# Kernel tuning notes

Measured on AMD Instinct MI355X. Metric: run time of the kernel, lower is better.

Reference implementation:

```python
import jax, jax.numpy as jnp
import numpy as np

HIDDEN = 1024
HEADS = 16
HEAD = HIDDEN // HEADS  # 64, rotary_emb_dim == head dim
B = 8
S = 1024  # max_seqlen; all sequences full length
WINDOW = (64, 64)  # sliding_window=128 -> (64, 64)
ROPE_BASE = 10000.0


def _rope_cos_sin(seqlen, dim, base):
    inv_freq = 1.0 / (base ** (jnp.arange(0, dim, 2, dtype=jnp.float32) / dim))
    t = jnp.arange(seqlen, dtype=jnp.float32)
    freqs = jnp.outer(t, inv_freq)  # [S, dim/2]
    return jnp.cos(freqs), jnp.sin(freqs)


def _apply_rope(x, cos, sin):
    # x: [B, S, H, D], non-interleaved rotary over full head dim
    d2 = cos.shape[-1]
    x1, x2 = x[..., :d2], x[..., d2:]
    c = cos[None, :, None, :]
    s = sin[None, :, None, :]
    return jnp.concatenate([x1 * c - x2 * s, x2 * c + x1 * s], axis=-1)


def setup_inputs() -> dict:
    key = jax.random.key(0)
    k1, k2, k3 = jax.random.split(key, 3)
    hidden_states = jax.random.normal(k1, (B * S, HIDDEN), dtype=jnp.float32)
    cu_seqlens = jnp.arange(B + 1, dtype=jnp.int32) * S
    indices = jnp.arange(B * S, dtype=jnp.int32)
    attn_mask = jnp.ones((B, S), dtype=jnp.int32)
    Wqkv = jax.random.normal(k2, (3 * HIDDEN, HIDDEN), dtype=jnp.float32) * 0.02
    Wo = jax.random.normal(k3, (HIDDEN, HIDDEN), dtype=jnp.float32) * 0.02
    return {
        'hidden_states': hidden_states,
        'cu_seqlens': cu_seqlens,
        'max_seqlen': S,
        'indices': indices,
        'attn_mask': attn_mask,
        'Wqkv': Wqkv,
        'Wo': Wo,
    }


def reference(hidden_states, cu_seqlens, max_seqlen, indices, attn_mask, Wqkv, Wo):
    # QKV projection on unpadded tokens: [T, 3*H*D]
    qkv = hidden_states @ Wqkv.T
    qkv = qkv.reshape(B, S, 3, HEADS, HEAD)
    # Rotary positions reset per sequence; all sequences are full length S.
    cos, sin = _rope_cos_sin(S, HEAD, ROPE_BASE)
    q = _apply_rope(qkv[:, :, 0], cos, sin)
    k = _apply_rope(qkv[:, :, 1], cos, sin)
    v = qkv[:, :, 2]
    scores = jnp.einsum('bshd,bthd->bhst', q, k) / jnp.sqrt(jnp.float32(HEAD))
    # sliding-window mask: key j visible to query i iff i-left <= j <= i+right
    i = jnp.arange(S)[:, None]
    j = jnp.arange(S)[None, :]
    win = (j >= i - WINDOW[0]) & (j <= i + WINDOW[1])  # [S, S]
    key_mask = attn_mask.astype(bool)[:, None, None, :]  # [B,1,1,S]
    mask = win[None, None, :, :] & key_mask
    scores = jnp.where(mask, scores, jnp.finfo(scores.dtype).min)
    probs = jax.nn.softmax(scores, axis=-1)
    attn = jnp.einsum('bhst,bthd->bshd', probs, v).reshape(B * S, HIDDEN)
    return attn @ Wo.T
```

## Files before the change

### kernel.cpp

```cpp
#include <hip/hip_runtime.h>


typedef __attribute__((ext_vector_type(8))) short short8;
typedef __attribute__((ext_vector_type(4))) float f32x4;

#define SEQ   1024
#define NHEAD 16
#define HEADD 64
#define NTOK  8192

__device__ __forceinline__ unsigned short f2bf(float x) {
  unsigned u = __float_as_uint(x);
  u += 0x7fffu + ((u >> 16) & 1u);
  return (unsigned short)(u >> 16);
}

__device__ __forceinline__ void gload_lds16(const void* g, void* l) {
  __builtin_amdgcn_global_load_lds((__attribute__((address_space(1))) void*)(g),
                                   (__attribute__((address_space(3))) void*)(l),
                                   16, 0, 0);
}

__global__ __launch_bounds__(256) void cvt_bf16(const float* __restrict__ in,
                                                unsigned short* __restrict__ out,
                                                int n4) {
  int i = blockIdx.x * 256 + threadIdx.x;
  if (i < n4) {
    float4 v = ((const float4*)in)[i];
    ushort4 o;
    o.x = f2bf(v.x); o.y = f2bf(v.y); o.z = f2bf(v.z); o.w = f2bf(v.w);
    ((ushort4*)out)[i] = o;
  }
}

__global__ __launch_bounds__(256) void gemm_qkv_rope(
    const unsigned short* __restrict__ A,
    const unsigned short* __restrict__ W,
    unsigned short* __restrict__ qb,
    unsigned short* __restrict__ kb,
    unsigned short* __restrict__ vt)
{
  __shared__ unsigned short As[128 * 32];
  __shared__ unsigned short Bs[128 * 32];
  const int tid  = threadIdx.x;
  const int wave = tid >> 6, lane = tid & 63;
  const int quad = lane >> 4, l15 = lane & 15;
  const int row0 = blockIdx.y * 128;
  const int col0 = blockIdx.x * 128;
  const int mrow = (wave >> 1) * 64;
  const int ncol = (wave & 1) * 64;

  f32x4 acc[4][4];
#pragma unroll
  for (int i = 0; i < 4; i++)
#pragma unroll
    for (int j = 0; j < 4; j++) acc[i][j] = (f32x4){0.f, 0.f, 0.f, 0.f};

  for (int k0 = 0; k0 < 1024; k0 += 32) {
#pragma unroll
    for (int i = 0; i < 2; i++) {
      int p = i * 256 + tid;
      int r = p >> 2, c = p & 3;
      gload_lds16(A + (size_t)(row0 + r) * 1024 + k0 + c * 8, &As[p * 8]);
      gload_lds16(W + (size_t)(col0 + r) * 1024 + k0 + c * 8, &Bs[p * 8]);
    }
    __syncthreads();
    short8 af[4], bf[4];
#pragma unroll
    for (int mt = 0; mt < 4; mt++)
      af[mt] = *(const short8*)&As[(mrow + mt * 16 + l15) * 32 + quad * 8];
#pragma unroll
    for (int nt = 0; nt < 4; nt++)
      bf[nt] = *(const short8*)&Bs[(ncol + nt * 16 + l15) * 32 + quad * 8];
#pragma unroll
    for (int mt = 0; mt < 4; mt++)
#pragma unroll
      for (int nt = 0; nt < 4; nt++)
        acc[mt][nt] = __builtin_amdgcn_mfma_f32_16x16x32_bf16(af[mt], bf[nt],
                                                              acc[mt][nt], 0, 0, 0);
    __syncthreads();
  }

  const int colw  = col0 + ncol;
  const int which = colw >> 10;
  const int h     = (colw >> 6) & 15;
  const int rowg  = row0 + mrow;

  if (which == 2) {
#pragma unroll
    for (int mt = 0; mt < 4; mt++) {
      int rbase = rowg + mt * 16 + quad * 4;
      int b = rbase >> 10, s = rbase & 1023;
#pragma unroll
      for (int c = 0; c < 4; c++) {
        int d = c * 16 + l15;
        ushort4 o;
        o.x = f2bf(acc[mt][c][0]); o.y = f2bf(acc[mt][c][1]);
        o.z = f2bf(acc[mt][c][2]); o.w = f2bf(acc[mt][c][3]);
        *(ushort4*)&vt[((size_t)((b * 16 + h) * 64 + d)) * 1024 + s] = o;
      }
    }
  } else {
    unsigned short* dst = (which == 0) ? qb : kb;
    const float scale = (which == 0) ? 0.125f : 1.0f;
    const float kf = 0.41524101186092034f;
    float inv0 = exp2f(-(float)l15 * kf);
    float inv1 = exp2f(-(float)(l15 + 16) * kf);
#pragma unroll
    for (int mt = 0; mt < 4; mt++) {
#pragma unroll
      for (int r = 0; r < 4; r++) {
        int row = rowg + mt * 16 + quad * 4 + r;
        int b = row >> 10, s = row & 1023;
        size_t base = (size_t)((b * 16 + h) * 1024 + s) * 64;
        float sn0, cs0, sn1, cs1;
        sincosf((float)s * inv0, &sn0, &cs0);
        sincosf((float)s * inv1, &sn1, &cs1);
        float x1a = acc[mt][0][r], x2a = acc[mt][2][r];
        float x1b = acc[mt][1][r], x2b = acc[mt][3][r];
        dst[base + l15]           = f2bf((x1a * cs0 - x2a * sn0) * scale);
        dst[base + 32 + l15]      = f2bf((x2a * cs0 + x1a * sn0) * scale);
        dst[base + 16 + l15]      = f2bf((x1b * cs1 - x2b * sn1) * scale);
        dst[base + 48 + l15]      = f2bf((x2b * cs1 + x1b * sn1) * scale);
      }
    }
  }
}

__global__ __launch_bounds__(256) void attn_win(
    const unsigned short* __restrict__ qb,
    const unsigned short* __restrict__ kb,
    const unsigned short* __restrict__ vt,
    const int* __restrict__ am,
    unsigned short* __restrict__ ob)
{
  __shared__ unsigned short Ks[192 * 72];
  __shared__ unsigned short Vs[64 * 200];
  __shared__ unsigned short Ps[4][16 * 200];
  __shared__ unsigned short smask[192];

  const int tid  = threadIdx.x;
  const int wave = tid >> 6, lane = tid & 63;
  const int quad = lane >> 4, l15 = lane & 15;
  const int qs = blockIdx.x * 64;
  const int h  = blockIdx.y, b = blockIdx.z;
  const size_t hb = (size_t)(b * 16 + h);
  const unsigned short* Qg = qb + hb * SEQ * 64;
  const unsigned short* Kg = kb + hb * SEQ * 64;
  const unsigned short* Vg = vt + hb * 64 * SEQ;
  const int t0 = qs - 64;

#pragma unroll
  for (int i = 0; i < 6; i++) {
    int p = i * 256 + tid;
    int r = p >> 3, c = p & 7;
    int t = t0 + r; t = t < 0 ? 0 : (t > 1023 ? 1023 : t);
    *(short8*)&Ks[r * 72 + c * 8] = *(const short8*)&Kg[(size_t)t * 64 + c * 8];
  }
#pragma unroll
  for (int i = 0; i < 6; i++) {
    int p = i * 256 + tid;
    int d = p / 24, c = p % 24;
    int t = t0 + c * 8; t = t < 0 ? 0 : (t > 1016 ? 1016 : t);
    *(short8*)&Vs[d * 200 + c * 8] = *(const short8*)&Vg[(size_t)d * SEQ + t];
  }
  if (tid < 192) {
    int t = t0 + tid;
    smask[tid] = (t >= 0 && t < SEQ) ? (unsigned short)(am[b * SEQ + t] != 0) : 0;
  }
  __syncthreads();

  const int qw = qs + wave * 16;
  short8 qf0 = *(const short8*)&Qg[(size_t)(qw + l15) * 64 + quad * 8];
  short8 qf1 = *(const short8*)&Qg[(size_t)(qw + l15) * 64 + 32 + quad * 8];

  f32x4 sc[12];
#pragma unroll
  for (int tt = 0; tt < 12; tt++) {
    short8 b0 = *(const short8*)&Ks[(tt * 16 + l15) * 72 + quad * 8];
    short8 b1 = *(const short8*)&Ks[(tt * 16 + l15) * 72 + 32 + quad * 8];
    f32x4 a = (f32x4){0.f, 0.f, 0.f, 0.f};
    a = __builtin_amdgcn_mfma_f32_16x16x32_bf16(qf0, b0, a, 0, 0, 0);
    a = __builtin_amdgcn_mfma_f32_16x16x32_bf16(qf1, b1, a, 0, 0, 0);
    sc[tt] = a;
  }

  float lrow[4];
#pragma unroll
  for (int r = 0; r < 4; r++) {
    int i = qw + quad * 4 + r;
    float mx = -3e38f;
#pragma unroll
    for (int tt = 0; tt < 12; tt++) {
      int t = t0 + tt * 16 + l15;
      bool ok = (t >= i - 64) && (t <= i + 64) && smask[tt * 16 + l15];
      float v = ok ? sc[tt][r] : -3e38f;
      sc[tt][r] = v;
      mx = fmaxf(mx, v);
    }
#pragma unroll
    for (int off = 1; off < 16; off <<= 1) mx = fmaxf(mx, __shfl_xor(mx, off));
    float sum = 0.f;
#pragma unroll
    for (int tt = 0; tt < 12; tt++) {
      float p = __expf(sc[tt][r] - mx);
      sc[tt][r] = p;
      sum += p;
    }
#pragma unroll
    for (int off = 1; off < 16; off <<= 1) sum += __shfl_xor(sum, off);
    lrow[r] = sum;
  }

  unsigned short* Pw = Ps[wave];
#pragma unroll
  for (int tt = 0; tt < 12; tt++)
#pragma unroll
    for (int r = 0; r < 4; r++)
      Pw[(quad * 4 + r) * 200 + tt * 16 + l15] = f2bf(sc[tt][r]);
  __syncthreads();

  f32x4 o[4];
#pragma unroll
  for (int dt = 0; dt < 4; dt++) o[dt] = (f32x4){0.f, 0.f, 0.f, 0.f};
#pragma unroll
  for (int kt = 0; kt < 6; kt++) {
    short8 pf = *(const short8*)&Pw[l15 * 200 + kt * 32 + quad * 8];
#pragma unroll
    for (int dt = 0; dt < 4; dt++) {
      short8 vf = *(const short8*)&Vs[(dt * 16 + l15) * 200 + kt * 32 + quad * 8];
      o[dt] = __builtin_amdgcn_mfma_f32_16x16x32_bf16(pf, vf, o[dt], 0, 0, 0);
    }
  }

#pragma unroll
  for (int r = 0; r < 4; r++) {
    float inv = 1.f / lrow[r];
    int tok = b * SEQ + qw + quad * 4 + r;
    size_t base = (size_t)tok * 1024 + h * 64;
#pragma unroll
    for (int dt = 0; dt < 4; dt++)
      ob[base + dt * 16 + l15] = f2bf(o[dt][r] * inv);
  }
}

__global__ __launch_bounds__(256) void gemm_out(
    const unsigned short* __restrict__ A,
    const unsigned short* __restrict__ W,
    float* __restrict__ out)
{
  __shared__ unsigned short As[128 * 32];
  __shared__ unsigned short Bs[128 * 32];
  const int tid  = threadIdx.x;
  const int wave = tid >> 6, lane = tid & 63;
  const int quad = lane >> 4, l15 = lane & 15;
  const int row0 = blockIdx.y * 128;
  const int col0 = blockIdx.x * 128;
  const int mrow = (wave >> 1) * 64;
  const int ncol = (wave & 1) * 64;

  f32x4 acc[4][4];
#pragma unroll
  for (int i = 0; i < 4; i++)
#pragma unroll
    for (int j = 0; j < 4; j++) acc[i][j] = (f32x4){0.f, 0.f, 0.f, 0.f};

  for (int k0 = 0; k0 < 1024; k0 += 32) {
#pragma unroll
    for (int i = 0; i < 2; i++) {
      int p = i * 256 + tid;
      int r = p >> 2, c = p & 3;
      gload_lds16(A + (size_t)(row0 + r) * 1024 + k0 + c * 8, &As[p * 8]);
      gload_lds16(W + (size_t)(col0 + r) * 1024 + k0 + c * 8, &Bs[p * 8]);
    }
    __syncthreads();
    short8 af[4], bf[4];
#pragma unroll
    for (int mt = 0; mt < 4; mt++)
      af[mt] = *(const short8*)&As[(mrow + mt * 16 + l15) * 32 + quad * 8];
#pragma unroll
    for (int nt = 0; nt < 4; nt++)
      bf[nt] = *(const short8*)&Bs[(ncol + nt * 16 + l15) * 32 + quad * 8];
#pragma unroll
    for (int mt = 0; mt < 4; mt++)
#pragma unroll
      for (int nt = 0; nt < 4; nt++)
        acc[mt][nt] = __builtin_amdgcn_mfma_f32_16x16x32_bf16(af[mt], bf[nt],
                                                              acc[mt][nt], 0, 0, 0);
    __syncthreads();
  }

  const int colw = col0 + ncol;
  const int rowg = row0 + mrow;
#pragma unroll
  for (int mt = 0; mt < 4; mt++)
#pragma unroll
    for (int r = 0; r < 4; r++) {
      int row = rowg + mt * 16 + quad * 4 + r;
#pragma unroll
      for (int nt = 0; nt < 4; nt++)
        out[(size_t)row * 1024 + colw + nt * 16 + l15] = acc[mt][nt][r];
    }
}

extern "C" void kernel_launch(void* const* d_in, const int* in_sizes, int n_in,
                              void* d_out, int out_size, void* d_ws, size_t ws_size,
                              hipStream_t stream) {
  const float* hidden = (const float*)d_in[0];
  const int*   am     = (const int*)d_in[4];
  const float* Wqkv   = (const float*)d_in[5];
  const float* Wo     = (const float*)d_in[6];
  float* out = (float*)d_out;

  char* ws = (char*)d_ws;
  unsigned short* hb  = (unsigned short*)(ws);
  unsigned short* wqb = (unsigned short*)(ws + (size_t)(16 << 20));
  unsigned short* wob = (unsigned short*)(ws + (size_t)(22 << 20));
  unsigned short* qbf = (unsigned short*)(ws + (size_t)(24 << 20));
  unsigned short* kbf = (unsigned short*)(ws + (size_t)(40 << 20));
  unsigned short* vtb = (unsigned short*)(ws + (size_t)(56 << 20));
  unsigned short* ab  = hb;

  cvt_bf16<<<(2097152 + 255) / 256, 256, 0, stream>>>(hidden, hb, 2097152);
  cvt_bf16<<<(786432 + 255) / 256, 256, 0, stream>>>(Wqkv, wqb, 786432);
  cvt_bf16<<<(262144 + 255) / 256, 256, 0, stream>>>(Wo, wob, 262144);

  dim3 g1(24, 64);
  gemm_qkv_rope<<<g1, 256, 0, stream>>>(hb, wqb, qbf, kbf, vtb);

  dim3 g2(16, 16, 8);
  attn_win<<<g2, 256, 0, stream>>>(qbf, kbf, vtb, am, ab);

  dim3 g3(8, 64);
  gemm_out<<<g3, 256, 0, stream>>>(ab, wob, out);
}
```

Measured before the change: 254.6 us.

## Merge bf16 conversion kernels and precompute RoPE cos/sin table

Combines the three float-to-bf16 conversion launches into one prep kernel. The same kernel also fills a per-position cos/sin table that the QKV GEMM epilogue reads instead of calling sincosf per element. This is meant to cut launch overhead and the expensive transcendental work in the RoPE epilogue. In exchange the epilogue does extra global loads of the 256KB table, which should mostly hit in cache.

```diff
diff --git a/kernel.cpp b/kernel.cpp
--- a/kernel.cpp
+++ b/kernel.cpp
@@ -21,21 +21,35 @@
                                    16, 0, 0);
 }
 
-__global__ __launch_bounds__(256) void cvt_bf16(const float* __restrict__ in,
-                                                unsigned short* __restrict__ out,
-                                                int n4) {
-  int i = blockIdx.x * 256 + threadIdx.x;
-  if (i < n4) {
-    float4 v = ((const float4*)in)[i];
-    ushort4 o;
-    o.x = f2bf(v.x); o.y = f2bf(v.y); o.z = f2bf(v.z); o.w = f2bf(v.w);
-    ((ushort4*)out)[i] = o;
-  }
+__global__ __launch_bounds__(256) void prep(
+    const float* __restrict__ hidden, const float* __restrict__ Wqkv,
+    const float* __restrict__ Wo,
+    unsigned short* __restrict__ hb, unsigned short* __restrict__ wqb,
+    unsigned short* __restrict__ wob, float2* __restrict__ tab) {
+  int bid = blockIdx.x;
+  const float* in; unsigned short* out; int i;
+  if (bid < 8192)       { in = hidden; out = hb;  i = bid * 256 + threadIdx.x; }
+  else if (bid < 11264) { in = Wqkv;   out = wqb; i = (bid - 8192) * 256 + threadIdx.x; }
+  else if (bid < 12288) { in = Wo;     out = wob; i = (bid - 11264) * 256 + threadIdx.x; }
+  else {
+    int j = (bid - 12288) * 256 + threadIdx.x;
+    int s = j >> 5, d = j & 31;
+    float inv = exp2f(-(float)d * 0.41524101186092034f);
+    float sn, cs;
+    sincosf((float)s * inv, &sn, &cs);
+    tab[j] = make_float2(cs, sn);
+    return;
+  }
+  float4 v = ((const float4*)in)[i];
+  ushort4 o;
+  o.x = f2bf(v.x); o.y = f2bf(v.y); o.z = f2bf(v.z); o.w = f2bf(v.w);
+  ((ushort4*)out)[i] = o;
 }
 
 __global__ __launch_bounds__(256) void gemm_qkv_rope(
     const unsigned short* __restrict__ A,
     const unsigned short* __restrict__ W,
+    const float2* __restrict__ tab,
     unsigned short* __restrict__ qb,
     unsigned short* __restrict__ kb,
     unsigned short* __restrict__ vt)
@@ -103,9 +117,6 @@
   } else {
     unsigned short* dst = (which == 0) ? qb : kb;
     const float scale = (which == 0) ? 0.125f : 1.0f;
-    const float kf = 0.41524101186092034f;
-    float inv0 = exp2f(-(float)l15 * kf);
-    float inv1 = exp2f(-(float)(l15 + 16) * kf);
 #pragma unroll
     for (int mt = 0; mt < 4; mt++) {
 #pragma unroll
@@ -113,15 +124,14 @@
         int row = rowg + mt * 16 + quad * 4 + r;
         int b = row >> 10, s = row & 1023;
         size_t base = (size_t)((b * 16 + h) * 1024 + s) * 64;
-        float sn0, cs0, sn1, cs1;
-        sincosf((float)s * inv0, &sn0, &cs0);
-        sincosf((float)s * inv1, &sn1, &cs1);
+        float2 t0 = tab[s * 32 + l15];
+        float2 t1 = tab[s * 32 + 16 + l15];
         float x1a = acc[mt][0][r], x2a = acc[mt][2][r];
         float x1b = acc[mt][1][r], x2b = acc[mt][3][r];
-        dst[base + l15]           = f2bf((x1a * cs0 - x2a * sn0) * scale);
-        dst[base + 32 + l15]      = f2bf((x2a * cs0 + x1a * sn0) * scale);
-        dst[base + 16 + l15]      = f2bf((x1b * cs1 - x2b * sn1) * scale);
-        dst[base + 48 + l15]      = f2bf((x2b * cs1 + x1b * sn1) * scale);
+        dst[base + l15]           = f2bf((x1a * t0.x - x2a * t0.y) * scale);
+        dst[base + 32 + l15]      = f2bf((x2a * t0.x + x1a * t0.y) * scale);
+        dst[base + 16 + l15]      = f2bf((x1b * t1.x - x2b * t1.y) * scale);
+        dst[base + 48 + l15]      = f2bf((x2b * t1.x + x1b * t1.y) * scale);
       }
     }
   }
@@ -319,14 +329,13 @@
   unsigned short* qbf = (unsigned short*)(ws + (size_t)(24 << 20));
   unsigned short* kbf = (unsigned short*)(ws + (size_t)(40 << 20));
   unsigned short* vtb = (unsigned short*)(ws + (size_t)(56 << 20));
+  float2*         tab = (float2*)(ws + (size_t)(72 << 20));
   unsigned short* ab  = hb;
 
-  cvt_bf16<<<(2097152 + 255) / 256, 256, 0, stream>>>(hidden, hb, 2097152);
-  cvt_bf16<<<(786432 + 255) / 256, 256, 0, stream>>>(Wqkv, wqb, 786432);
-  cvt_bf16<<<(262144 + 255) / 256, 256, 0, stream>>>(Wo, wob, 262144);
+  prep<<<12416, 256, 0, stream>>>(hidden, Wqkv, Wo, hb, wqb, wob, tab);
 
   dim3 g1(24, 64);
-  gemm_qkv_rope<<<g1, 256, 0, stream>>>(hb, wqb, qbf, kbf, vtb);
+  gemm_qkv_rope<<<g1, 256, 0, stream>>>(hb, wqb, tab, qbf, kbf, vtb);
 
   dim3 g2(16, 16, 8);
   attn_win<<<g2, 256, 0, stream>>>(qbf, kbf, vtb, am, ab);
```

New measurement: 247.4 us. -2.8%, faster.
